# Kernel optimization log

Measured on AMD Instinct MI355X. Metric: run time of the kernel, lower is better.

The kernel has to match this reference:

```python
import jax, jax.numpy as jnp
from jax import lax
import numpy as np

V, B, T, H = 8000, 64, 128, 512
MAXC = 10          # max pondering steps (ACT max_computation)
EPS = 0.01         # ACT epsilon
PONDER_PEN = 0.01  # ponder_time_penalty


def setup_inputs() -> dict:
    key = jax.random.key(0)
    ks = jax.random.split(key, 10)
    return {
        "input_data": jax.random.randint(ks[0], (B, T), 0, V),
        "embedding": jax.random.uniform(ks[1], (V, H), minval=-1.0, maxval=1.0, dtype=jnp.float32),
        # GRU weights; cell input = [embedded char (H), ACT binary flag (1)] -> input dim H+1
        "W_gates": jax.random.normal(ks[2], (2 * H + 1, 2 * H), dtype=jnp.float32) * 0.05,
        "b_gates": jnp.ones((2 * H,), jnp.float32),  # TF GRUCell gate bias init 1.0
        "W_cand": jax.random.normal(ks[3], (2 * H + 1, H), dtype=jnp.float32) * 0.05,
        "b_cand": jnp.zeros((H,), jnp.float32),
        "w_halt": jax.random.normal(ks[4], (H,), dtype=jnp.float32) * 0.05,
        "b_halt": jnp.ones((), jnp.float32),
        "softmax_w": jax.random.normal(ks[5], (V, H), dtype=jnp.float32) * 0.02,
        "softmax_b": jnp.zeros((V,), jnp.float32),
    }


def _gru(inp, h, Wg, bg, Wc, bc):
    # TF GRUCell: r,u = sigmoid([x,h]Wg + bg); c = tanh([x, r*h]Wc + bc); h' = u*h + (1-u)*c
    xh = jnp.concatenate([inp, h], axis=-1)
    r, u = jnp.split(jax.nn.sigmoid(xh @ Wg + bg), 2, axis=-1)
    c = jnp.tanh(jnp.concatenate([inp, r * h], axis=-1) @ Wc + bc)
    return u * h + (1.0 - u) * c


def _act_timestep(h0, x, Wg, bg, Wc, bc, w_halt, b_halt):
    # One ACT-wrapped timestep: masked fixed-length pondering loop (equivalent math
    # to the data-dependent halting loop; steps after halting have zero weight).
    zero = jnp.zeros((B,), jnp.float32)

    def inner(carry, i):
        h, acc, cum_p, remainder, n_upd = carry
        still = cum_p < (1.0 - EPS)                       # [B] elements still pondering
        flag = jnp.where(i == 0, 1.0, 0.0) * jnp.ones((B, 1), jnp.float32)
        h_new = _gru(jnp.concatenate([x, flag], axis=-1), h, Wg, bg, Wc, bc)
        p = jax.nn.sigmoid(h_new @ w_halt + b_halt)       # [B] halting prob
        is_last = i == (MAXC - 1)
        halts_now = still & ((cum_p + p >= 1.0 - EPS) | is_last)
        w = jnp.where(halts_now, 1.0 - cum_p, p) * still.astype(jnp.float32)
        acc = acc + w[:, None] * h_new                    # weighted-mean output/state
        remainder = jnp.where(halts_now, 1.0 - cum_p, remainder)
        n_upd = n_upd + still.astype(jnp.float32)
        h = jnp.where(still[:, None], h_new, h)
        cum_p = cum_p + p * still.astype(jnp.float32)
        return (h, acc, cum_p, remainder, n_upd), None

    init = (h0, jnp.zeros_like(h0), zero, zero, zero)
    (h, acc, cum_p, remainder, n_upd), _ = lax.scan(inner, init, jnp.arange(MAXC))
    ponder = n_upd + remainder                            # [B]
    return acc, ponder


def reference(input_data, embedding, W_gates, b_gates, W_cand, b_cand,
              w_halt, b_halt, softmax_w, softmax_b):
    x = embedding[input_data]                             # [B,T,H]

    def step(h, xt):
        out, ponder = _act_timestep(h, xt, W_gates, b_gates, W_cand, b_cand, w_halt, b_halt)
        return out, (out, ponder)                         # ACT state == weighted output

    h0 = jnp.zeros((B, H), jnp.float32)
    _, (outs, ponders) = lax.scan(step, h0, jnp.swapaxes(x, 0, 1))  # outs [T,B,H]
    outs = jnp.swapaxes(outs, 0, 1).reshape(-1, H)        # [B*T,H] batch-major like TF reshape
    logits = outs @ softmax_w.T + softmax_b               # [B*T,V]
    ponder_cost = PONDER_PEN * jnp.mean(jnp.sum(ponders, axis=0))
    return logits, ponder_cost
```

## Files before the change

### kernel.cpp

```cpp
#include <hip/hip_runtime.h>
#include <math.h>

#define BB 64
#define TT 128
#define HH 512
#define VV 8000
#define MAXC 10
#define GBLK 32
#define RTHREADS 512

typedef short short8 __attribute__((ext_vector_type(8)));
typedef float floatx4 __attribute__((ext_vector_type(4)));

__device__ __forceinline__ float sigmoidf_(float x) { return 1.0f / (1.0f + __expf(-x)); }
__device__ __forceinline__ unsigned short f2bf(float x) {
    unsigned int u = __float_as_uint(x);
    unsigned int r = u + 0x7FFFu + ((u >> 16) & 1u);
    return (unsigned short)(r >> 16);
}
__device__ __forceinline__ float bf2f(unsigned short h) {
    return __uint_as_float(((unsigned int)h) << 16);
}

__device__ __forceinline__ void gbar(unsigned int* cnt, int s) {
    __syncthreads();
    if (threadIdx.x == 0) {
        __threadfence();
        unsigned int* c = cnt + s;
        __hip_atomic_fetch_add(c, 1u, __ATOMIC_RELEASE, __HIP_MEMORY_SCOPE_AGENT);
        while (__hip_atomic_load(c, __ATOMIC_ACQUIRE, __HIP_MEMORY_SCOPE_AGENT) < GBLK) {}
        __threadfence();
    }
    __syncthreads();
}

__global__ __launch_bounds__(256) void transpose_w(
    const float* __restrict__ Wg, const float* __restrict__ Wc,
    unsigned short* __restrict__ WgT, unsigned short* __restrict__ WcT)
{
    __shared__ float tile[64][65];
    int bid = blockIdx.x;
    const float* src; unsigned short* dst; int N, n0, k0;
    if (bid < 128) { src = Wg + (size_t)513 * 1024; dst = WgT; N = 1024;
                     n0 = (bid & 15) * 64; k0 = (bid >> 4) * 64; }
    else { bid -= 128; src = Wc + (size_t)513 * 512; dst = WcT; N = 512;
           n0 = (bid & 7) * 64; k0 = (bid >> 3) * 64; }
    const int tid = threadIdx.x;
    const int nn = tid & 63, kb = tid >> 6;
#pragma unroll
    for (int p = 0; p < 16; ++p) {
        int kk = kb + p * 4;
        tile[kk][nn] = src[(size_t)(k0 + kk) * N + n0 + nn];
    }
    __syncthreads();
    const int kk2 = tid & 63;
#pragma unroll
    for (int p = 0; p < 16; ++p) {
        int nn2 = kb + p * 4;
        dst[(size_t)(n0 + nn2) * 512 + k0 + kk2] = f2bf(tile[kk2][nn2]);
    }
}

__global__ __launch_bounds__(256) void xproj_kernel(
    const int* __restrict__ idx, const float* __restrict__ emb,
    const float* __restrict__ W, const float* __restrict__ bias,
    float* __restrict__ outf, unsigned short* __restrict__ outb, int N)
{
    __shared__ float As[16][68];
    __shared__ float Bs[16][68];
    __shared__ int rows[64];
    const int tn0 = blockIdx.x * 64, tm0 = blockIdx.y * 64;
    const int tid = threadIdx.x;
    if (tid < 64) rows[tid] = idx[tm0 + tid];
    __syncthreads();

    float acc[4][4] = {};
    const int am = tid >> 2, ak = (tid & 3) * 4;
    const int bk = tid >> 4, bn = (tid & 15) * 4;
    const int tm = (tid >> 4) * 4, tn = (tid & 15) * 4;

    for (int k0 = 0; k0 < HH; k0 += 16) {
        const float4 av = *(const float4*)(emb + (size_t)rows[am] * HH + k0 + ak);
        As[ak + 0][am] = av.x; As[ak + 1][am] = av.y;
        As[ak + 2][am] = av.z; As[ak + 3][am] = av.w;
        *(float4*)&Bs[bk][bn] = *(const float4*)(W + (size_t)(k0 + bk) * N + tn0 + bn);
        __syncthreads();
#pragma unroll
        for (int k = 0; k < 16; ++k) {
            float a[4], b[4];
#pragma unroll
            for (int i = 0; i < 4; ++i) a[i] = As[k][tm + i];
#pragma unroll
            for (int i = 0; i < 4; ++i) b[i] = Bs[k][tn + i];
#pragma unroll
            for (int i = 0; i < 4; ++i)
#pragma unroll
                for (int j = 0; j < 4; ++j) acc[i][j] += a[i] * b[j];
        }
        __syncthreads();
    }
#pragma unroll
    for (int i = 0; i < 4; ++i) {
        int r = tm0 + tm + i;
        size_t orow = (size_t)((r % TT) * 64 + r / TT);
#pragma unroll
        for (int j = 0; j < 4; ++j) {
            float v = acc[i][j] + bias[tn0 + tn + j];
            if (outb) outb[orow * N + tn0 + tn + j] = f2bf(v);
            else      outf[orow * N + tn0 + tn + j] = v;
        }
    }
}

__global__ __launch_bounds__(RTHREADS) void act_rnn_batched(
    const unsigned short* __restrict__ WgT, const unsigned short* __restrict__ WcT,
    const float* __restrict__ Wg, const float* __restrict__ Wc,
    const float* __restrict__ whalt, const float* __restrict__ bhalt,
    const unsigned short* __restrict__ Xg, const float* __restrict__ Xc,
    float* __restrict__ outs, float* __restrict__ ponder_b,
    unsigned short* __restrict__ RHX, unsigned short* __restrict__ HNX,
    unsigned short* __restrict__ AccX, float* __restrict__ Pp,
    unsigned int* __restrict__ cnt)
{
    __shared__ unsigned short Hs[64][520];
    __shared__ unsigned short Wgl[32][520];
    __shared__ unsigned short Wcl[16][520];
    __shared__ float u_l[64][16];
    __shared__ float pl[64][17];
    __shared__ float w_s[64], cum_s[64], rem_s[64], nupd_s[64], pond_s[64];
    __shared__ int still_s[64];
    __shared__ int allh_s;
    __shared__ float fg_l[32], fc_l[16], wh_l[16];

    const int tid = threadIdx.x;
    const int g = blockIdx.x;
    const int wv = tid >> 6, lane = tid & 63, l15 = lane & 15, quad = lane >> 4;
    const int mt = wv & 3, nt = wv >> 2;

    {
        int row = tid >> 4;
        int c0 = (tid & 15) * 32;
        int src_n = (row < 16) ? (16 * g + row) : (512 + 16 * g + (row - 16));
        const unsigned short* s = WgT + (size_t)src_n * 512 + c0;
        unsigned short* d = &Wgl[row][c0];
#pragma unroll
        for (int q = 0; q < 4; ++q) ((uint4*)d)[q] = ((const uint4*)s)[q];
    }
    if (tid < 256) {
        int row = tid >> 4;
        int c0 = (tid & 15) * 32;
        const unsigned short* s = WcT + (size_t)(16 * g + row) * 512 + c0;
        unsigned short* d = &Wcl[row][c0];
#pragma unroll
        for (int q = 0; q < 4; ++q) ((uint4*)d)[q] = ((const uint4*)s)[q];
    }
    if (tid < 32) fg_l[tid] = Wg[(size_t)512 * 1024 +
                                 ((tid < 16) ? (16 * g + tid) : (512 + 16 * g + tid - 16))];
    if (tid < 16) { fc_l[tid] = Wc[(size_t)512 * 512 + 16 * g + tid];
                    wh_l[tid] = whalt[16 * g + tid]; }
    for (int x = tid; x < 64 * 520; x += RTHREADS) ((unsigned short*)Hs)[x] = 0;
    if (tid < 64) { cum_s[tid] = 0; rem_s[tid] = 0; nupd_s[tid] = 0; pond_s[tid] = 0; }
    const float bh = bhalt[0];
    __syncthreads();

    int seq = 0;
    floatx4 accr = {0, 0, 0, 0};
    float hn[4] = {0, 0, 0, 0};

    for (int t = 0; t < TT; ++t) {
        for (int i = 0; i < MAXC; ++i) {
            floatx4 acg = {0, 0, 0, 0};
            const int arow = mt * 16 + l15;
            const int brow = nt * 16 + l15;
#pragma unroll
            for (int kk = 0; kk < 16; ++kk) {
                short8 a = *(const short8*)&Hs[arow][kk * 32 + quad * 8];
                short8 b = *(const short8*)&Wgl[brow][kk * 32 + quad * 8];
                acg = __builtin_amdgcn_mfma_f32_16x16x32_bf16(a, b, acg, 0, 0, 0);
            }
            const int gcol = (nt == 0) ? (16 * g + l15) : (512 + 16 * g + l15);
#pragma unroll
            for (int e = 0; e < 4; ++e) {
                int m = mt * 16 + quad * 4 + e;
                float pre = acg[e] + bf2f(Xg[(size_t)(t * 64 + m) * 1024 + gcol])
                            + ((i == 0) ? fg_l[nt * 16 + l15] : 0.0f);
                float s = sigmoidf_(pre);
                if (nt == 0) {
                    float rh = s * bf2f(Hs[m][16 * g + l15]);
                    RHX[(size_t)m * 512 + 16 * g + l15] = f2bf(rh);
                } else {
                    u_l[m][l15] = s;
                }
            }
            gbar(cnt, seq++);

            if (wv < 4) {
                short8 af[16];
#pragma unroll
                for (int kk = 0; kk < 16; ++kk)
                    af[kk] = *(const short8*)&RHX[(size_t)(mt * 16 + l15) * 512 + kk * 32 + quad * 8];
                floatx4 ac2 = {0, 0, 0, 0};
#pragma unroll
                for (int kk = 0; kk < 16; ++kk) {
                    short8 b = *(const short8*)&Wcl[l15][kk * 32 + quad * 8];
                    ac2 = __builtin_amdgcn_mfma_f32_16x16x32_bf16(af[kk], b, ac2, 0, 0, 0);
                }
#pragma unroll
                for (int e = 0; e < 4; ++e) {
                    int m = mt * 16 + quad * 4 + e;
                    int j = 16 * g + l15;
                    float pre = ac2[e] + Xc[(size_t)(t * 64 + m) * 512 + j]
                                + ((i == 0) ? fc_l[l15] : 0.0f);
                    float c = tanhf(pre);
                    float u = u_l[m][l15];
                    float h = bf2f(Hs[m][j]);
                    hn[e] = u * h + (1.0f - u) * c;
                    HNX[(size_t)m * 512 + j] = f2bf(hn[e]);
                    pl[m][l15] = hn[e] * wh_l[l15];
                }
            }
            __syncthreads();
            if (tid < 64) {
                float s = 0.0f;
#pragma unroll
                for (int j = 0; j < 16; ++j) s += pl[tid][j];
                Pp[g * 64 + tid] = s;
            }
            gbar(cnt, seq++);

            if (tid < 64) {
                float logit = bh;
                for (int gg = 0; gg < GBLK; ++gg) logit += Pp[gg * 64 + tid];
                float p = sigmoidf_(logit);
                float cum = cum_s[tid];
                bool still = cum < 0.99f;
                bool halts = still && ((cum + p >= 0.99f) || (i == MAXC - 1));
                w_s[tid] = still ? (halts ? (1.0f - cum) : p) : 0.0f;
                still_s[tid] = still ? 1 : 0;
                if (halts) rem_s[tid] = 1.0f - cum;
                if (still) { nupd_s[tid] += 1.0f; cum_s[tid] = cum + p; }
                unsigned long long act = __ballot(still && !halts);
                if (tid == 0) allh_s = (act == 0ull) ? 1 : 0;
            }
            __syncthreads();
            if (wv < 4) {
#pragma unroll
                for (int e = 0; e < 4; ++e) {
                    int m = mt * 16 + quad * 4 + e;
                    accr[e] += w_s[m] * hn[e];
                }
            }
            {
                int row = tid >> 3;
                int c0 = (tid & 7) * 64;
                if (still_s[row]) {
                    const uint4* s = (const uint4*)&HNX[(size_t)row * 512 + c0];
                    uint4* d = (uint4*)&Hs[row][c0];
#pragma unroll
                    for (int q = 0; q < 8; ++q) d[q] = s[q];
                }
            }
            __syncthreads();
            if (allh_s) break;
        }

        if (wv < 4) {
#pragma unroll
            for (int e = 0; e < 4; ++e) {
                int m = mt * 16 + quad * 4 + e;
                int j = 16 * g + l15;
                outs[(size_t)(m * TT + t) * 512 + j] = accr[e];
                AccX[(size_t)m * 512 + j] = f2bf(accr[e]);
                accr[e] = 0.0f;
            }
        }
        if (tid < 64) {
            pond_s[tid] += nupd_s[tid] + rem_s[tid];
            cum_s[tid] = 0; rem_s[tid] = 0; nupd_s[tid] = 0;
        }
        gbar(cnt, seq++);
        {
            int row = tid >> 3;
            int c0 = (tid & 7) * 64;
            const uint4* s = (const uint4*)&AccX[(size_t)row * 512 + c0];
            uint4* d = (uint4*)&Hs[row][c0];
#pragma unroll
            for (int q = 0; q < 8; ++q) d[q] = s[q];
        }
        __syncthreads();
    }
    if (g == 0 && tid < 64) ponder_b[tid] = pond_s[tid];
}

__global__ __launch_bounds__(256) void logits_kernel(
    const float* __restrict__ Amat, const float* __restrict__ sw,
    const float* __restrict__ sb, float* __restrict__ out)
{
    __shared__ float As[16][68];
    __shared__ float Bs[16][68];
    const int tn0 = blockIdx.x * 64, tm0 = blockIdx.y * 64;
    const int tid = threadIdx.x;

    float acc[4][4] = {};
    const int am = tid >> 2, ak = (tid & 3) * 4;
    const int bn_ = tid >> 2, bkq = (tid & 3) * 4;
    const int tm = (tid >> 4) * 4, tn = (tid & 15) * 4;

    for (int k0 = 0; k0 < HH; k0 += 16) {
        const float4 av = *(const float4*)(Amat + (size_t)(tm0 + am) * HH + k0 + ak);
        As[ak + 0][am] = av.x; As[ak + 1][am] = av.y;
        As[ak + 2][am] = av.z; As[ak + 3][am] = av.w;
        const float4 bv = *(const float4*)(sw + (size_t)(tn0 + bn_) * HH + k0 + bkq);
        Bs[bkq + 0][bn_] = bv.x; Bs[bkq + 1][bn_] = bv.y;
        Bs[bkq + 2][bn_] = bv.z; Bs[bkq + 3][bn_] = bv.w;
        __syncthreads();
#pragma unroll
        for (int k = 0; k < 16; ++k) {
            float a[4], b[4];
#pragma unroll
            for (int i = 0; i < 4; ++i) a[i] = As[k][tm + i];
#pragma unroll
            for (int i = 0; i < 4; ++i) b[i] = Bs[k][tn + i];
#pragma unroll
            for (int i = 0; i < 4; ++i)
#pragma unroll
                for (int j = 0; j < 4; ++j) acc[i][j] += a[i] * b[j];
        }
        __syncthreads();
    }
#pragma unroll
    for (int i = 0; i < 4; ++i)
#pragma unroll
        for (int j = 0; j < 4; ++j)
            out[(size_t)(tm0 + tm + i) * VV + tn0 + tn + j] = acc[i][j] + sb[tn0 + tn + j];
}

__global__ void ponder_kernel(const float* __restrict__ pb, float* __restrict__ out,
                              unsigned long long off)
{
    const int lane = threadIdx.x;
    float v = pb[lane];
#pragma unroll
    for (int o = 32; o > 0; o >>= 1) v += __shfl_down(v, o, 64);
    if (lane == 0) out[off] = 0.01f * (v * (1.0f / 64.0f));
}

extern "C" void kernel_launch(void* const* d_in, const int* in_sizes, int n_in,
                              void* d_out, int out_size, void* d_ws, size_t ws_size,
                              hipStream_t stream)
{
    const int*   idx = (const int*)d_in[0];
    const float* emb = (const float*)d_in[1];
    const float* Wg  = (const float*)d_in[2];
    const float* bg  = (const float*)d_in[3];
    const float* Wc  = (const float*)d_in[4];
    const float* bc  = (const float*)d_in[5];
    const float* wh  = (const float*)d_in[6];
    const float* bh  = (const float*)d_in[7];
    const float* sw  = (const float*)d_in[8];
    const float* sb  = (const float*)d_in[9];
    float* out = (float*)d_out;

    float* ws   = (float*)d_ws;
    float* Xc   = ws;
    float* outs = Xc + (size_t)8192 * 512;
    float* pb   = outs + (size_t)8192 * 512;
    float* Pp   = pb + 64;
    unsigned int* cnt = (unsigned int*)(Pp + 2048);
    unsigned short* Xg  = (unsigned short*)(cnt + 4096);
    unsigned short* WgT = Xg + (size_t)8192 * 1024;
    unsigned short* WcT = WgT + (size_t)1024 * 512;
    unsigned short* RHX = WcT + (size_t)512 * 512;
    unsigned short* HNX = RHX + (size_t)64 * 512;
    unsigned short* AccX = HNX + (size_t)64 * 512;

    hipMemsetAsync(cnt, 0, 4096 * sizeof(unsigned int), stream);
    transpose_w<<<192, 256, 0, stream>>>(Wg, Wc, WgT, WcT);
    xproj_kernel<<<dim3(16, 128), 256, 0, stream>>>(idx, emb, Wg, bg, nullptr, Xg, 1024);
    xproj_kernel<<<dim3(8, 128), 256, 0, stream>>>(idx, emb, Wc, bc, Xc, nullptr, 512);
    act_rnn_batched<<<GBLK, RTHREADS, 0, stream>>>(WgT, WcT, Wg, Wc, wh, bh, Xg, Xc,
                                                   outs, pb, RHX, HNX, AccX, Pp, cnt);
    logits_kernel<<<dim3(VV / 64, 128), 256, 0, stream>>>(outs, sw, sb, out);
    ponder_kernel<<<1, 64, 0, stream>>>(pb, out, (unsigned long long)8192 * VV);
}
```

Before: 5.718 ms.

## Replace atomic-counter barrier with flag barrier, stage inputs in LDS, MFMA logits

The grid barrier changes from a per-step atomic counter that one thread spins on to per-block sequence flags that one wavefront polls with a ballot. Cross-block exchanges now use relaxed atomic 8-byte loads and stores instead of fences. Per-timestep Xg and Xc slices are staged into LDS once rather than re-read from global memory in every pondering step. The fp32 logits GEMM becomes a bf16 MFMA GEMM over a bf16 copy of the softmax weights and bf16 RNN outputs, which adds a conversion kernel and lowers output precision. Dropping the fences relies on relaxed atomics staying coherent across blocks, which risks memory-ordering bugs.

```diff
diff --git a/kernel.cpp b/kernel.cpp
--- a/kernel.cpp
+++ b/kernel.cpp
@@ -11,6 +11,7 @@
 
 typedef short short8 __attribute__((ext_vector_type(8)));
 typedef float floatx4 __attribute__((ext_vector_type(4)));
+typedef unsigned long long u64;
 
 __device__ __forceinline__ float sigmoidf_(float x) { return 1.0f / (1.0f + __expf(-x)); }
 __device__ __forceinline__ unsigned short f2bf(float x) {
@@ -22,14 +23,29 @@
     return __uint_as_float(((unsigned int)h) << 16);
 }
 
-__device__ __forceinline__ void gbar(unsigned int* cnt, int s) {
+__device__ __forceinline__ u64 ald8(const unsigned short* p) {
+    return __hip_atomic_load((const u64*)p, __ATOMIC_RELAXED, __HIP_MEMORY_SCOPE_AGENT);
+}
+__device__ __forceinline__ void ast8(unsigned short* p, u64 v) {
+    __hip_atomic_store((u64*)p, v, __ATOMIC_RELAXED, __HIP_MEMORY_SCOPE_AGENT);
+}
+__device__ __forceinline__ short8 ald16(const unsigned short* p) {
+    union { short8 v; u64 q[2]; } u;
+    u.q[0] = ald8(p); u.q[1] = ald8(p + 4);
+    return u.v;
+}
+
+__device__ __forceinline__ void xbar(unsigned int* flags, unsigned int seq) {
     __syncthreads();
-    if (threadIdx.x == 0) {
-        __threadfence();
-        unsigned int* c = cnt + s;
-        __hip_atomic_fetch_add(c, 1u, __ATOMIC_RELEASE, __HIP_MEMORY_SCOPE_AGENT);
-        while (__hip_atomic_load(c, __ATOMIC_ACQUIRE, __HIP_MEMORY_SCOPE_AGENT) < GBLK) {}
-        __threadfence();
+    if (threadIdx.x == 0)
+        __hip_atomic_store(flags + blockIdx.x, seq, __ATOMIC_RELAXED, __HIP_MEMORY_SCOPE_AGENT);
+    if (threadIdx.x < 64) {
+        unsigned int f = seq;
+        do {
+            if (threadIdx.x < GBLK)
+                f = __hip_atomic_load(flags + threadIdx.x, __ATOMIC_RELAXED,
+                                      __HIP_MEMORY_SCOPE_AGENT);
+        } while (__ballot(f < seq) != 0ull);
     }
     __syncthreads();
 }
@@ -117,15 +133,19 @@
     const float* __restrict__ Wg, const float* __restrict__ Wc,
     const float* __restrict__ whalt, const float* __restrict__ bhalt,
     const unsigned short* __restrict__ Xg, const float* __restrict__ Xc,
-    float* __restrict__ outs, float* __restrict__ ponder_b,
+    unsigned short* __restrict__ outsb, float* __restrict__ ponder_b,
     unsigned short* __restrict__ RHX, unsigned short* __restrict__ HNX,
     unsigned short* __restrict__ AccX, float* __restrict__ Pp,
-    unsigned int* __restrict__ cnt)
+    unsigned int* __restrict__ flags)
 {
     __shared__ unsigned short Hs[64][520];
     __shared__ unsigned short Wgl[32][520];
     __shared__ unsigned short Wcl[16][520];
+    __shared__ unsigned short xg_l[64][32];
+    __shared__ float xc_l[64][16];
     __shared__ float u_l[64][16];
+    __shared__ float rh_l[64][16];
+    __shared__ float hn_l[64][16];
     __shared__ float pl[64][17];
     __shared__ float w_s[64], cum_s[64], rem_s[64], nupd_s[64], pond_s[64];
     __shared__ int still_s[64];
@@ -163,11 +183,22 @@
     const float bh = bhalt[0];
     __syncthreads();
 
-    int seq = 0;
+    unsigned int seq = 0;
     floatx4 accr = {0, 0, 0, 0};
     float hn[4] = {0, 0, 0, 0};
 
     for (int t = 0; t < TT; ++t) {
+        {
+            int row = tid >> 3, cc = (tid & 7) * 4;
+            int gcol = (cc < 16) ? (16 * g + cc) : (512 + 16 * g + (cc - 16));
+            *(u64*)&xg_l[row][cc] = *(const u64*)(Xg + (size_t)(t * 64 + row) * 1024 + gcol);
+        }
+        if (tid < 256) {
+            int row = tid >> 2, c4 = (tid & 3) * 4;
+            *(float4*)&xc_l[row][c4] = *(const float4*)(Xc + (size_t)(t * 64 + row) * 512 + 16 * g + c4);
+        }
+        __syncthreads();
+
         for (int i = 0; i < MAXC; ++i) {
             floatx4 acg = {0, 0, 0, 0};
             const int arow = mt * 16 + l15;
@@ -178,27 +209,31 @@
                 short8 b = *(const short8*)&Wgl[brow][kk * 32 + quad * 8];
                 acg = __builtin_amdgcn_mfma_f32_16x16x32_bf16(a, b, acg, 0, 0, 0);
             }
-            const int gcol = (nt == 0) ? (16 * g + l15) : (512 + 16 * g + l15);
 #pragma unroll
             for (int e = 0; e < 4; ++e) {
                 int m = mt * 16 + quad * 4 + e;
-                float pre = acg[e] + bf2f(Xg[(size_t)(t * 64 + m) * 1024 + gcol])
+                float pre = acg[e] + bf2f(xg_l[m][nt * 16 + l15])
                             + ((i == 0) ? fg_l[nt * 16 + l15] : 0.0f);
                 float s = sigmoidf_(pre);
-                if (nt == 0) {
-                    float rh = s * bf2f(Hs[m][16 * g + l15]);
-                    RHX[(size_t)m * 512 + 16 * g + l15] = f2bf(rh);
-                } else {
-                    u_l[m][l15] = s;
-                }
-            }
-            gbar(cnt, seq++);
+                if (nt == 0) rh_l[m][l15] = s * bf2f(Hs[m][16 * g + l15]);
+                else         u_l[m][l15] = s;
+            }
+            __syncthreads();
+            if (tid < 256) {
+                int row = tid >> 2, q = tid & 3;
+                u64 v = (u64)f2bf(rh_l[row][q * 4 + 0])
+                      | ((u64)f2bf(rh_l[row][q * 4 + 1]) << 16)
+                      | ((u64)f2bf(rh_l[row][q * 4 + 2]) << 32)
+                      | ((u64)f2bf(rh_l[row][q * 4 + 3]) << 48);
+                ast8(RHX + (size_t)row * 512 + 16 * g + q * 4, v);
+            }
+            xbar(flags, ++seq);
 
             if (wv < 4) {
                 short8 af[16];
 #pragma unroll
                 for (int kk = 0; kk < 16; ++kk)
-                    af[kk] = *(const short8*)&RHX[(size_t)(mt * 16 + l15) * 512 + kk * 32 + quad * 8];
+                    af[kk] = ald16(RHX + (size_t)(mt * 16 + l15) * 512 + kk * 32 + quad * 8);
                 floatx4 ac2 = {0, 0, 0, 0};
 #pragma unroll
                 for (int kk = 0; kk < 16; ++kk) {
@@ -208,29 +243,39 @@
 #pragma unroll
                 for (int e = 0; e < 4; ++e) {
                     int m = mt * 16 + quad * 4 + e;
-                    int j = 16 * g + l15;
-                    float pre = ac2[e] + Xc[(size_t)(t * 64 + m) * 512 + j]
-                                + ((i == 0) ? fc_l[l15] : 0.0f);
+                    float pre = ac2[e] + xc_l[m][l15] + ((i == 0) ? fc_l[l15] : 0.0f);
                     float c = tanhf(pre);
                     float u = u_l[m][l15];
-                    float h = bf2f(Hs[m][j]);
+                    float h = bf2f(Hs[m][16 * g + l15]);
                     hn[e] = u * h + (1.0f - u) * c;
-                    HNX[(size_t)m * 512 + j] = f2bf(hn[e]);
+                    hn_l[m][l15] = hn[e];
                     pl[m][l15] = hn[e] * wh_l[l15];
                 }
             }
             __syncthreads();
+            if (tid < 256) {
+                int row = tid >> 2, q = tid & 3;
+                u64 v = (u64)f2bf(hn_l[row][q * 4 + 0])
+                      | ((u64)f2bf(hn_l[row][q * 4 + 1]) << 16)
+                      | ((u64)f2bf(hn_l[row][q * 4 + 2]) << 32)
+                      | ((u64)f2bf(hn_l[row][q * 4 + 3]) << 48);
+                ast8(HNX + (size_t)row * 512 + 16 * g + q * 4, v);
+            }
             if (tid < 64) {
                 float s = 0.0f;
 #pragma unroll
                 for (int j = 0; j < 16; ++j) s += pl[tid][j];
-                Pp[g * 64 + tid] = s;
-            }
-            gbar(cnt, seq++);
+                __hip_atomic_store(Pp + g * 64 + tid, s, __ATOMIC_RELAXED,
+                                   __HIP_MEMORY_SCOPE_AGENT);
+            }
+            xbar(flags, ++seq);
 
             if (tid < 64) {
                 float logit = bh;
-                for (int gg = 0; gg < GBLK; ++gg) logit += Pp[gg * 64 + tid];
+#pragma unroll
+                for (int gg = 0; gg < GBLK; ++gg)
+                    logit += __hip_atomic_load(Pp + gg * 64 + tid, __ATOMIC_RELAXED,
+                                               __HIP_MEMORY_SCOPE_AGENT);
                 float p = sigmoidf_(logit);
                 float cum = cum_s[tid];
                 bool still = cum < 0.99f;
@@ -251,13 +296,12 @@
                 }
             }
             {
-                int row = tid >> 3;
-                int c0 = (tid & 7) * 64;
+                int row = tid >> 3, c0s = (tid & 7) * 64;
                 if (still_s[row]) {
-                    const uint4* s = (const uint4*)&HNX[(size_t)row * 512 + c0];
-                    uint4* d = (uint4*)&Hs[row][c0];
-#pragma unroll
-                    for (int q = 0; q < 8; ++q) d[q] = s[q];
+                    const unsigned short* s = HNX + (size_t)row * 512 + c0s;
+#pragma unroll
+                    for (int q = 0; q < 16; ++q)
+                        *(u64*)&Hs[row][c0s + q * 4] = ald8(s + q * 4);
                 }
             }
             __syncthreads();
@@ -269,70 +313,93 @@
             for (int e = 0; e < 4; ++e) {
                 int m = mt * 16 + quad * 4 + e;
                 int j = 16 * g + l15;
-                outs[(size_t)(m * TT + t) * 512 + j] = accr[e];
-                AccX[(size_t)m * 512 + j] = f2bf(accr[e]);
+                unsigned short ab = f2bf(accr[e]);
+                outsb[(size_t)(m * TT + t) * 512 + j] = ab;
+                rh_l[m][l15] = accr[e];
                 accr[e] = 0.0f;
             }
+        }
+        __syncthreads();
+        if (tid < 256) {
+            int row = tid >> 2, q = tid & 3;
+            u64 v = (u64)f2bf(rh_l[row][q * 4 + 0])
+                  | ((u64)f2bf(rh_l[row][q * 4 + 1]) << 16)
+                  | ((u64)f2bf(rh_l[row][q * 4 + 2]) << 32)
+                  | ((u64)f2bf(rh_l[row][q * 4 + 3]) << 48);
+            ast8(AccX + (size_t)row * 512 + 16 * g + q * 4, v);
         }
         if (tid < 64) {
             pond_s[tid] += nupd_s[tid] + rem_s[tid];
             cum_s[tid] = 0; rem_s[tid] = 0; nupd_s[tid] = 0;
         }
-        gbar(cnt, seq++);
+        xbar(flags, ++seq);
         {
-            int row = tid >> 3;
-            int c0 = (tid & 7) * 64;
-            const uint4* s = (const uint4*)&AccX[(size_t)row * 512 + c0];
-            uint4* d = (uint4*)&Hs[row][c0];
-#pragma unroll
-            for (int q = 0; q < 8; ++q) d[q] = s[q];
+            int row = tid >> 3, c0s = (tid & 7) * 64;
+            const unsigned short* s = AccX + (size_t)row * 512 + c0s;
+#pragma unroll
+            for (int q = 0; q < 16; ++q)
+                *(u64*)&Hs[row][c0s + q * 4] = ald8(s + q * 4);
         }
         __syncthreads();
     }
     if (g == 0 && tid < 64) ponder_b[tid] = pond_s[tid];
 }
 
-__global__ __launch_bounds__(256) void logits_kernel(
-    const float* __restrict__ Amat, const float* __restrict__ sw,
+__global__ __launch_bounds__(256) void cvt_bf16(
+    const float* __restrict__ s, unsigned short* __restrict__ d)
+{
+    int i = (blockIdx.x * 256 + threadIdx.x) * 4;
+    float4 v = *(const float4*)(s + i);
+    u64 p = (u64)f2bf(v.x) | ((u64)f2bf(v.y) << 16)
+          | ((u64)f2bf(v.z) << 32) | ((u64)f2bf(v.w) << 48);
+    *(u64*)(d + i) = p;
+}
+
+__global__ __launch_bounds__(256) void logits_mfma(
+    const unsigned short* __restrict__ A,
+    const unsigned short* __restrict__ Bw,
     const float* __restrict__ sb, float* __restrict__ out)
 {
-    __shared__ float As[16][68];
-    __shared__ float Bs[16][68];
-    const int tn0 = blockIdx.x * 64, tm0 = blockIdx.y * 64;
+    __shared__ unsigned short As[128][40];
+    __shared__ unsigned short Bs[64][40];
+    const int n0 = blockIdx.x * 64, m0 = blockIdx.y * 128;
     const int tid = threadIdx.x;
-
-    float acc[4][4] = {};
-    const int am = tid >> 2, ak = (tid & 3) * 4;
-    const int bn_ = tid >> 2, bkq = (tid & 3) * 4;
-    const int tm = (tid >> 4) * 4, tn = (tid & 15) * 4;
-
-    for (int k0 = 0; k0 < HH; k0 += 16) {
-        const float4 av = *(const float4*)(Amat + (size_t)(tm0 + am) * HH + k0 + ak);
-        As[ak + 0][am] = av.x; As[ak + 1][am] = av.y;
-        As[ak + 2][am] = av.z; As[ak + 3][am] = av.w;
-        const float4 bv = *(const float4*)(sw + (size_t)(tn0 + bn_) * HH + k0 + bkq);
-        Bs[bkq + 0][bn_] = bv.x; Bs[bkq + 1][bn_] = bv.y;
-        Bs[bkq + 2][bn_] = bv.z; Bs[bkq + 3][bn_] = bv.w;
-        __syncthreads();
-#pragma unroll
-        for (int k = 0; k < 16; ++k) {
-            float a[4], b[4];
-#pragma unroll
-            for (int i = 0; i < 4; ++i) a[i] = As[k][tm + i];
-#pragma unroll
-            for (int i = 0; i < 4; ++i) b[i] = Bs[k][tn + i];
-#pragma unroll
-            for (int i = 0; i < 4; ++i)
-#pragma unroll
-                for (int j = 0; j < 4; ++j) acc[i][j] += a[i] * b[j];
-        }
-        __syncthreads();
-    }
-#pragma unroll
-    for (int i = 0; i < 4; ++i)
-#pragma unroll
-        for (int j = 0; j < 4; ++j)
-            out[(size_t)(tm0 + tm + i) * VV + tn0 + tn + j] = acc[i][j] + sb[tn0 + tn + j];
+    const int wv = tid >> 6, lane = tid & 63, l15 = lane & 15, quad = lane >> 4;
+
+    floatx4 acc[2][4] = {};
+    for (int k0 = 0; k0 < HH; k0 += 32) {
+#pragma unroll
+        for (int c = tid; c < 512; c += 256) {
+            int r = c >> 2, q = c & 3;
+            *(uint4*)&As[r][q * 8] = *(const uint4*)(A + (size_t)(m0 + r) * 512 + k0 + q * 8);
+        }
+        {
+            int n = tid >> 2, q = tid & 3;
+            *(uint4*)&Bs[n][q * 8] = *(const uint4*)(Bw + (size_t)(n0 + n) * 512 + k0 + q * 8);
+        }
+        __syncthreads();
+        short8 b[4];
+#pragma unroll
+        for (int nb = 0; nb < 4; ++nb) b[nb] = *(const short8*)&Bs[nb * 16 + l15][quad * 8];
+#pragma unroll
+        for (int r = 0; r < 2; ++r) {
+            short8 a = *(const short8*)&As[wv * 32 + r * 16 + l15][quad * 8];
+#pragma unroll
+            for (int nb = 0; nb < 4; ++nb)
+                acc[r][nb] = __builtin_amdgcn_mfma_f32_16x16x32_bf16(a, b[nb], acc[r][nb], 0, 0, 0);
+        }
+        __syncthreads();
+    }
+#pragma unroll
+    for (int r = 0; r < 2; ++r)
+#pragma unroll
+        for (int nb = 0; nb < 4; ++nb)
+#pragma unroll
+            for (int e = 0; e < 4; ++e) {
+                int row = m0 + wv * 32 + r * 16 + quad * 4 + e;
+                int col = n0 + nb * 16 + l15;
+                out[(size_t)row * VV + col] = acc[r][nb][e] + sb[col];
+            }
 }
 
 __global__ void ponder_kernel(const float* __restrict__ pb, float* __restrict__ out,
@@ -361,25 +428,27 @@
     const float* sb  = (const float*)d_in[9];
     float* out = (float*)d_out;
 
-    float* ws   = (float*)d_ws;
-    float* Xc   = ws;
-    float* outs = Xc + (size_t)8192 * 512;
-    float* pb   = outs + (size_t)8192 * 512;
-    float* Pp   = pb + 64;
-    unsigned int* cnt = (unsigned int*)(Pp + 2048);
-    unsigned short* Xg  = (unsigned short*)(cnt + 4096);
-    unsigned short* WgT = Xg + (size_t)8192 * 1024;
-    unsigned short* WcT = WgT + (size_t)1024 * 512;
-    unsigned short* RHX = WcT + (size_t)512 * 512;
-    unsigned short* HNX = RHX + (size_t)64 * 512;
-    unsigned short* AccX = HNX + (size_t)64 * 512;
-
-    hipMemsetAsync(cnt, 0, 4096 * sizeof(unsigned int), stream);
+    char* p = (char*)d_ws;
+    unsigned int* flags = (unsigned int*)p;      p += 256;
+    float* Xc  = (float*)p;                      p += (size_t)8192 * 512 * 4;
+    float* pb  = (float*)p;                      p += 256;
+    float* Pp  = (float*)p;                      p += (size_t)GBLK * 64 * 4;
+    unsigned short* Xg    = (unsigned short*)p;  p += (size_t)8192 * 1024 * 2;
+    unsigned short* WgT   = (unsigned short*)p;  p += (size_t)1024 * 512 * 2;
+    unsigned short* WcT   = (unsigned short*)p;  p += (size_t)512 * 512 * 2;
+    unsigned short* RHX   = (unsigned short*)p;  p += (size_t)64 * 512 * 2;
+    unsigned short* HNX   = (unsigned short*)p;  p += (size_t)64 * 512 * 2;
+    unsigned short* AccX  = (unsigned short*)p;  p += (size_t)64 * 512 * 2;
+    unsigned short* outsb = (unsigned short*)p;  p += (size_t)8192 * 512 * 2;
+    unsigned short* swb   = (unsigned short*)p;  p += (size_t)VV * 512 * 2;
+
+    hipMemsetAsync(flags, 0, 256, stream);
     transpose_w<<<192, 256, 0, stream>>>(Wg, Wc, WgT, WcT);
     xproj_kernel<<<dim3(16, 128), 256, 0, stream>>>(idx, emb, Wg, bg, nullptr, Xg, 1024);
     xproj_kernel<<<dim3(8, 128), 256, 0, stream>>>(idx, emb, Wc, bc, Xc, nullptr, 512);
+    cvt_bf16<<<(VV * 512) / 1024, 256, 0, stream>>>(sw, swb);
     act_rnn_batched<<<GBLK, RTHREADS, 0, stream>>>(WgT, WcT, Wg, Wc, wh, bh, Xg, Xc,
-                                                   outs, pb, RHX, HNX, AccX, Pp, cnt);
-    logits_kernel<<<dim3(VV / 64, 128), 256, 0, stream>>>(outs, sw, sb, out);
+                                                   outsb, pb, RHX, HNX, AccX, Pp, flags);
+    logits_mfma<<<dim3(VV / 64, 64), 256, 0, stream>>>(outsb, swb, sb, out);
     ponder_kernel<<<1, 64, 0, stream>>>(pb, out, (unsigned long long)8192 * VV);
 }
```

Result: faster. 4.743 ms (-17.0%).
